# Performance work log

Measured on AMD Instinct MI355X. Metric: run time of the kernel, lower is better.

## Reference

```python
import jax, jax.numpy as jnp
import numpy as np

NUM_EMBEDDINGS = 1024
EMBEDDING_DIM = 64
COMMITMENT_COST = 0.25


def setup_inputs() -> dict:
    key = jax.random.key(0)
    k1, k2 = jax.random.split(key)
    inputs = jax.random.normal(k1, (8, 128, 128, EMBEDDING_DIM), dtype=jnp.float32)
    # nn.Embedding init: uniform(-1/K, 1/K)
    codebook = jax.random.uniform(
        k2, (NUM_EMBEDDINGS, EMBEDDING_DIM), dtype=jnp.float32,
        minval=-1.0 / NUM_EMBEDDINGS, maxval=1.0 / NUM_EMBEDDINGS)
    return {"inputs": inputs, "codebook": codebook}


def reference(inputs, codebook):
    input_shape = inputs.shape
    flat = inputs.reshape(-1, EMBEDDING_DIM)  # [N, D]
    distances = (jnp.sum(flat * flat, axis=1, keepdims=True)
                 + jnp.sum(codebook * codebook, axis=1)
                 - 2.0 * jnp.matmul(flat, codebook.T))  # [N, K]
    encoding_indices = jnp.argmin(distances, axis=1)  # [N]
    # one-hot @ codebook == direct gather
    quantized = codebook[encoding_indices].reshape(input_shape)
    e_latent_loss = jnp.mean((jax.lax.stop_gradient(quantized) - inputs) ** 2)
    q_latent_loss = jnp.mean((quantized - jax.lax.stop_gradient(inputs)) ** 2)
    vq_loss = q_latent_loss + COMMITMENT_COST * e_latent_loss
    # straight-through estimator
    quantized = inputs + jax.lax.stop_gradient(quantized - inputs)
    return (quantized, vq_loss, encoding_indices[:, None])
```

## Files before the change

### kernel.cpp

```cpp
#include <hip/hip_runtime.h>


typedef _Float16 f16x8 __attribute__((ext_vector_type(8)));
typedef float f32x4 __attribute__((ext_vector_type(4)));

constexpr int Dm = 64;
constexpr int Kn = 1024;
constexpr long NR = 131072;
constexpr long QE = NR * (long)Dm;
constexpr int RB = 64;
constexpr int NBLK = (int)(NR / RB);
constexpr int CH = 64;
constexpr int NCH = Kn / CH;
constexpr int SP4 = 17;

constexpr size_t SE_OFF   = 0;
constexpr size_t CBH_OFF  = 4096;
constexpr size_t CNT_OFF  = CBH_OFF + 131072;
constexpr size_t HARD_OFF = CNT_OFF + 256;
constexpr size_t RL_OFF   = HARD_OFF + 4 * 131072;
constexpr size_t PART_OFF = RL_OFF + 4 * 131072;
constexpr size_t WS_REQ   = PART_OFF + 4096;

__global__ __launch_bounds__(256) void vq_prep(const float* __restrict__ cb,
                                               float* __restrict__ se,
                                               _Float16* __restrict__ cbh,
                                               int* __restrict__ cnt)
{
    int j = blockIdx.x * 256 + threadIdx.x;
    const float* e = cb + (size_t)j * Dm;
    _Float16* h = cbh + (size_t)j * Dm;
    float s = 0.f;
    #pragma unroll
    for (int d = 0; d < Dm; ++d) s = fmaf(e[d], e[d], s);
    se[j] = s;
    #pragma unroll
    for (int d = 0; d < Dm; ++d) h[d] = (_Float16)(e[d] * 1024.0f);
    if (j == 0) *cnt = 0;
}

__global__ __launch_bounds__(256, 4) void vq_pass1(
    const float* __restrict__ inp, const float* __restrict__ cb,
    const _Float16* __restrict__ cbh, const float* __restrict__ seg,
    float* __restrict__ out, int* __restrict__ hard_list, int* __restrict__ cnt,
    float* __restrict__ row_loss)
{
    __shared__ __align__(16) _Float16 xh[RB * 72];
    __shared__ float se[Kn];
    __shared__ float gs[RB];
    __shared__ float wm1[4][RB], wm2[4][RB];
    __shared__ int   wi1[4][RB];
    __shared__ int   ridx[RB];
    __shared__ int   easyf[RB];
    __shared__ double qd[RB][4];

    const int tid = threadIdx.x;
    const long rbase = (long)blockIdx.x * RB;

    #pragma unroll
    for (int k = 0; k < 4; ++k) se[tid + 256 * k] = seg[tid + 256 * k];

    {
        const int r = tid >> 2, q = tid & 3;
        const float* src = inp + (rbase + r) * Dm + q * 16;
        _Float16* dst = xh + r * 72 + q * 16;
        #pragma unroll
        for (int i = 0; i < 4; ++i) {
            float4 v = *reinterpret_cast<const float4*>(src + 4 * i);
            dst[4*i+0] = (_Float16)v.x; dst[4*i+1] = (_Float16)v.y;
            dst[4*i+2] = (_Float16)v.z; dst[4*i+3] = (_Float16)v.w;
        }
    }
    if (tid < RB) {
        const float* xr = inp + (rbase + tid) * Dm;
        float g = 0.f;
        #pragma unroll
        for (int d = 0; d < Dm; ++d) g += fabsf(xr[d]);
        gs[tid] = g;
    }
    __syncthreads();

    const int w = tid >> 6, l = tid & 63;
    const int arow = l & 15, kg = l >> 4;

    f16x8 a0[4], a1[4];
    #pragma unroll
    for (int rt = 0; rt < 4; ++rt) {
        const _Float16* ap = xh + (rt * 16 + arow) * 72 + kg * 8;
        a0[rt] = *reinterpret_cast<const f16x8*>(ap);
        a1[rt] = *reinterpret_cast<const f16x8*>(ap + 32);
    }

    float mn1[4][4], mn2[4][4]; int ix1[4][4];
    #pragma unroll
    for (int rt = 0; rt < 4; ++rt)
        #pragma unroll
        for (int r = 0; r < 4; ++r) {
            mn1[rt][r] = __builtin_inff(); mn2[rt][r] = __builtin_inff();
            ix1[rt][r] = 0;
        }

    const int code0 = w * 256 + arow;
    const _Float16* bp = cbh + (size_t)code0 * Dm + kg * 8;

    f16x8 b0 = *reinterpret_cast<const f16x8*>(bp);
    f16x8 b1 = *reinterpret_cast<const f16x8*>(bp + 32);
    #pragma unroll 2
    for (int t = 0; t < 16; ++t) {
        f16x8 c0 = b0, c1 = b1;
        const _Float16* tpn = bp + ((t + 1) & 15) * 16 * Dm;
        b0 = *reinterpret_cast<const f16x8*>(tpn);
        b1 = *reinterpret_cast<const f16x8*>(tpn + 32);
        const int code = code0 + t * 16;
        const float sec = se[code];
        #pragma unroll
        for (int rt = 0; rt < 4; ++rt) {
            f32x4 acc = {0.f, 0.f, 0.f, 0.f};
            acc = __builtin_amdgcn_mfma_f32_16x16x32_f16(a0[rt], c0, acc, 0, 0, 0);
            acc = __builtin_amdgcn_mfma_f32_16x16x32_f16(a1[rt], c1, acc, 0, 0, 0);
            #pragma unroll
            for (int r = 0; r < 4; ++r) {
                float m = fmaf(acc[r], -0.001953125f, sec);
                mn2[rt][r] = fminf(mn2[rt][r], fmaxf(mn1[rt][r], m));
                ix1[rt][r] = (m < mn1[rt][r]) ? code : ix1[rt][r];
                mn1[rt][r] = fminf(mn1[rt][r], m);
            }
        }
    }

    #pragma unroll
    for (int rt = 0; rt < 4; ++rt)
        #pragma unroll
        for (int r = 0; r < 4; ++r) {
            float m1v = mn1[rt][r], m2v = mn2[rt][r]; int i1v = ix1[rt][r];
            #pragma unroll
            for (int off = 1; off < 16; off <<= 1) {
                float om1 = __shfl_xor(m1v, off);
                float om2 = __shfl_xor(m2v, off);
                int   oi1 = __shfl_xor(i1v, off);
                float nm2 = fminf(fminf(m2v, om2), fmaxf(m1v, om1));
                i1v = (om1 < m1v) ? oi1 : i1v;
                m1v = fminf(m1v, om1);
                m2v = nm2;
            }
            if (arow == 0) {
                const int row = rt * 16 + kg * 4 + r;
                wm1[w][row] = m1v; wm2[w][row] = m2v; wi1[w][row] = i1v;
            }
        }
    __syncthreads();

    if (tid < RB) {
        float m1v = wm1[0][tid], m2v = wm2[0][tid]; int i1v = wi1[0][tid];
        #pragma unroll
        for (int q = 1; q < 4; ++q) {
            float am1 = wm1[q][tid], am2 = wm2[q][tid]; int ai = wi1[q][tid];
            float nm2 = fminf(fminf(m2v, am2), fmaxf(m1v, am1));
            i1v = (am1 < m1v) ? ai : i1v;
            m1v = fminf(m1v, am1);
            m2v = nm2;
        }
        const float T = fmaf(gs[tid], 5.2e-6f, 4.0e-5f);
        const int easy = (m2v - m1v) > T;
        ridx[tid] = i1v;
        easyf[tid] = easy;
        if (easy) out[QE + 1 + rbase + tid] = (float)i1v;
        unsigned long long hm = __ballot(!easy);
        const int nh = __popcll(hm);
        int base = 0;
        if (tid == 0 && nh) base = atomicAdd(cnt, nh);
        base = __shfl(base, 0);
        if (!easy) {
            const int pos = base + __popcll(hm & ((1ull << tid) - 1ull));
            hard_list[pos] = (int)(rbase + tid);
        }
    }
    __syncthreads();

    const int r2 = tid >> 2;
    const int dq = (tid & 3) * 16;
    if (easyf[r2]) {
        const long grow = rbase + r2;
        const float* xr2 = inp + grow * (long)Dm + dq;
        const float* q2  = cb + (size_t)ridx[r2] * Dm + dq;
        float* outq = out + grow * (long)Dm + dq;
        double s = 0.0;
        #pragma unroll
        for (int d0 = 0; d0 < 16; d0 += 4) {
            float4 xv = *reinterpret_cast<const float4*>(xr2 + d0);
            float4 qv = *reinterpret_cast<const float4*>(q2 + d0);
            float4 ov;
            float m0 = qv.x - xv.x; ov.x = xv.x + m0;
            float m1 = qv.y - xv.y; ov.y = xv.y + m1;
            float m2 = qv.z - xv.z; ov.z = xv.z + m2;
            float m3 = qv.w - xv.w; ov.w = xv.w + m3;
            s += (double)m0*m0 + (double)m1*m1 + (double)m2*m2 + (double)m3*m3;
            *reinterpret_cast<float4*>(outq + d0) = ov;
        }
        qd[r2][tid & 3] = s;
    }
    __syncthreads();
    if (tid < RB && easyf[tid]) {
        double s = qd[tid][0] + qd[tid][1] + qd[tid][2] + qd[tid][3];
        row_loss[rbase + tid] = (float)s;
    }
}

__global__ __launch_bounds__(256) void vq_pass2(
    const float* __restrict__ inp, const float* __restrict__ cb,
    const float* __restrict__ seg, float* __restrict__ out,
    const int* __restrict__ hard_list, const int* __restrict__ cnt,
    float* __restrict__ row_loss)
{
    __shared__ float4 xs[RB * SP4];
    __shared__ float4 es[CH * SP4];
    __shared__ float  ses[Kn];
    __shared__ float  sxs[RB];
    __shared__ int    hr[RB];
    __shared__ float  bd[RB * 17];
    __shared__ int    bi[RB * 17];
    __shared__ int    comb[RB];
    __shared__ double qd[RB][4];

    const int tid = threadIdx.x;
    const int tr = tid & 15;
    const int tc = tid >> 4;

    #pragma unroll
    for (int k = 0; k < 4; ++k) ses[tid + 256 * k] = seg[tid + 256 * k];

    const int total = *cnt;
    const int nchunk = (total + RB - 1) / RB;
    const float4* gcb = reinterpret_cast<const float4*>(cb);

    for (int c = blockIdx.x; c < nchunk; c += gridDim.x) {
        __syncthreads();
        if (tid < RB) {
            int gi = c * RB + tid;
            hr[tid] = (gi < total) ? hard_list[gi] : -1;
        }
        __syncthreads();

        #pragma unroll
        for (int r = 0; r < 4; ++r) {
            int g = r * 256 + tid;
            int row = g >> 4, col = g & 15;
            int gr = hr[row];
            float4 v = {0.f, 0.f, 0.f, 0.f};
            if (gr >= 0)
                v = *reinterpret_cast<const float4*>(inp + (size_t)gr * Dm + col * 4);
            xs[row * SP4 + col] = v;
        }
        __syncthreads();

        if (tid < RB) {
            const float* xr = reinterpret_cast<const float*>(&xs[tid * SP4]);
            float s = 0.f;
            #pragma unroll
            for (int d = 0; d < Dm; ++d) s = fmaf(xr[d], xr[d], s);
            sxs[tid] = s;
        }
        __syncthreads();

        float sxr[4];
        #pragma unroll
        for (int rr = 0; rr < 4; ++rr) sxr[rr] = sxs[tr + 16 * rr];

        float best[4]; int bidx[4];
        #pragma unroll
        for (int rr = 0; rr < 4; ++rr) { best[rr] = __builtin_inff(); bidx[rr] = 0; }

        for (int ch = 0; ch < NCH; ++ch) {
            __syncthreads();
            #pragma unroll
            for (int r = 0; r < 4; ++r) {
                int g = r * 256 + tid;
                es[(g >> 4) * SP4 + (g & 15)] = gcb[(size_t)ch * (CH * Dm / 4) + g];
            }
            __syncthreads();

            float acc[4][4];
            #pragma unroll
            for (int rr = 0; rr < 4; ++rr)
                #pragma unroll
                for (int cc = 0; cc < 4; ++cc) acc[rr][cc] = 0.f;

            #pragma unroll 4
            for (int db = 0; db < 16; ++db) {
                float4 xf[4], ef[4];
                #pragma unroll
                for (int rr = 0; rr < 4; ++rr) xf[rr] = xs[(tr + 16 * rr) * SP4 + db];
                #pragma unroll
                for (int cc = 0; cc < 4; ++cc) ef[cc] = es[(tc + 16 * cc) * SP4 + db];
                #pragma unroll
                for (int rr = 0; rr < 4; ++rr)
                    #pragma unroll
                    for (int cc = 0; cc < 4; ++cc) {
                        float a = acc[rr][cc];
                        a = fmaf(xf[rr].x, ef[cc].x, a);
                        a = fmaf(xf[rr].y, ef[cc].y, a);
                        a = fmaf(xf[rr].z, ef[cc].z, a);
                        a = fmaf(xf[rr].w, ef[cc].w, a);
                        acc[rr][cc] = a;
                    }
            }

            const int cbase = ch * CH;
            #pragma unroll
            for (int cc = 0; cc < 4; ++cc) {
                const int code = cbase + tc + 16 * cc;
                const float sec = ses[code];
                #pragma unroll
                for (int rr = 0; rr < 4; ++rr) {
                    float dist = (sxr[rr] + sec) - 2.0f * acc[rr][cc];
                    if (dist < best[rr]) { best[rr] = dist; bidx[rr] = code; }
                }
            }
        }

        #pragma unroll
        for (int rr = 0; rr < 4; ++rr) {
            int row = tr + 16 * rr;
            bd[row * 17 + tc] = best[rr];
            bi[row * 17 + tc] = bidx[rr];
        }
        __syncthreads();

        if (tid < RB && hr[tid] >= 0) {
            float b = bd[tid * 17]; int ii = bi[tid * 17];
            #pragma unroll
            for (int q = 1; q < 16; ++q) {
                float d = bd[tid * 17 + q]; int iq = bi[tid * 17 + q];
                if (d < b || (d == b && iq < ii)) { b = d; ii = iq; }
            }
            comb[tid] = ii;
            out[QE + 1 + hr[tid]] = (float)ii;
        }
        __syncthreads();

        const int r2 = tid >> 2;
        const int dq = (tid & 3) * 16;
        if (hr[r2] >= 0) {
            const long grow = hr[r2];
            const float* xr2 = inp + grow * (long)Dm + dq;
            const float* q2  = cb + (size_t)comb[r2] * Dm + dq;
            float* outq = out + grow * (long)Dm + dq;
            double s = 0.0;
            #pragma unroll
            for (int d0 = 0; d0 < 16; d0 += 4) {
                float4 xv = *reinterpret_cast<const float4*>(xr2 + d0);
                float4 qv = *reinterpret_cast<const float4*>(q2 + d0);
                float4 ov;
                float m0 = qv.x - xv.x; ov.x = xv.x + m0;
                float m1 = qv.y - xv.y; ov.y = xv.y + m1;
                float m2 = qv.z - xv.z; ov.z = xv.z + m2;
                float m3 = qv.w - xv.w; ov.w = xv.w + m3;
                s += (double)m0*m0 + (double)m1*m1 + (double)m2*m2 + (double)m3*m3;
                *reinterpret_cast<float4*>(outq + d0) = ov;
            }
            qd[r2][tid & 3] = s;
        }
        __syncthreads();
        if (tid < RB && hr[tid] >= 0) {
            double s = qd[tid][0] + qd[tid][1] + qd[tid][2] + qd[tid][3];
            row_loss[hr[tid]] = (float)s;
        }
    }
}

__global__ __launch_bounds__(256) void vq_lred(const float* __restrict__ row_loss,
                                               double* __restrict__ part)
{
    __shared__ double red[256];
    const int tid = threadIdx.x;
    red[tid] = (double)row_loss[(size_t)blockIdx.x * 256 + tid];
    __syncthreads();
    for (int k = 128; k > 0; k >>= 1) {
        if (tid < k) red[tid] += red[tid + k];
        __syncthreads();
    }
    if (tid == 0) part[blockIdx.x] = red[0];
}

__global__ __launch_bounds__(256) void vq_fin(const double* __restrict__ part,
                                              float* __restrict__ out)
{
    __shared__ double red[256];
    const int tid = threadIdx.x;
    red[tid] = part[tid] + part[tid + 256];
    __syncthreads();
    for (int k = 128; k > 0; k >>= 1) {
        if (tid < k) red[tid] += red[tid + k];
        __syncthreads();
    }
    if (tid == 0) {
        float m = (float)(red[0] / (double)QE);
        out[QE] = m + 0.25f * m;
    }
}

extern "C" void kernel_launch(void* const* d_in, const int* in_sizes, int n_in,
                              void* d_out, int out_size, void* d_ws, size_t ws_size,
                              hipStream_t stream)
{
    const float* inp = (const float*)d_in[0];
    const float* cb  = (const float*)d_in[1];
    float* out = (float*)d_out;
    char* ws = (char*)d_ws;

    float*    se   = (float*)(ws + SE_OFF);
    _Float16* cbh  = (_Float16*)(ws + CBH_OFF);
    int*      cnt  = (int*)(ws + CNT_OFF);
    int*      hard = (int*)(ws + HARD_OFF);
    float*    rl   = (float*)(ws + RL_OFF);
    double*   part = (double*)(ws + PART_OFF);

    vq_prep<<<4, 256, 0, stream>>>(cb, se, cbh, cnt);
    vq_pass1<<<NBLK, 256, 0, stream>>>(inp, cb, cbh, se, out, hard, cnt, rl);
    vq_pass2<<<512, 256, 0, stream>>>(inp, cb, se, out, hard, cnt, rl);
    vq_lred<<<512, 256, 0, stream>>>(rl, part);
    vq_fin<<<1, 256, 0, stream>>>(part, out);
}
```

Measured before the change: 141.5 us.

## Split codebook into fp16 hi/lo parts to tighten pass-1 distance error

The codebook is now stored as a high fp16 part plus a residual low fp16 part, and pass 1 issues two extra MFMAs per tile to add the residual contribution. This halves the approximation error, so the easy/hard margin threshold is halved and fewer rows should fall through to the exact fp32 pass 2. In exchange pass 1 does twice the MFMA work and twice the codebook loads, and it drops the software prefetch of the next B tile.

```diff
diff --git a/kernel.cpp b/kernel.cpp
--- a/kernel.cpp
+++ b/kernel.cpp
@@ -16,7 +16,8 @@
 
 constexpr size_t SE_OFF   = 0;
 constexpr size_t CBH_OFF  = 4096;
-constexpr size_t CNT_OFF  = CBH_OFF + 131072;
+constexpr size_t CBL_OFF  = CBH_OFF + 131072;
+constexpr size_t CNT_OFF  = CBL_OFF + 131072;
 constexpr size_t HARD_OFF = CNT_OFF + 256;
 constexpr size_t RL_OFF   = HARD_OFF + 4 * 131072;
 constexpr size_t PART_OFF = RL_OFF + 4 * 131072;
@@ -25,24 +26,32 @@
 __global__ __launch_bounds__(256) void vq_prep(const float* __restrict__ cb,
                                                float* __restrict__ se,
                                                _Float16* __restrict__ cbh,
+                                               _Float16* __restrict__ cbl,
                                                int* __restrict__ cnt)
 {
     int j = blockIdx.x * 256 + threadIdx.x;
     const float* e = cb + (size_t)j * Dm;
     _Float16* h = cbh + (size_t)j * Dm;
+    _Float16* l = cbl + (size_t)j * Dm;
     float s = 0.f;
     #pragma unroll
     for (int d = 0; d < Dm; ++d) s = fmaf(e[d], e[d], s);
     se[j] = s;
     #pragma unroll
-    for (int d = 0; d < Dm; ++d) h[d] = (_Float16)(e[d] * 1024.0f);
+    for (int d = 0; d < Dm; ++d) {
+        float sc = e[d] * 1024.0f;
+        _Float16 hh = (_Float16)sc;
+        h[d] = hh;
+        l[d] = (_Float16)(sc - (float)hh);
+    }
     if (j == 0) *cnt = 0;
 }
 
 __global__ __launch_bounds__(256, 4) void vq_pass1(
     const float* __restrict__ inp, const float* __restrict__ cb,
-    const _Float16* __restrict__ cbh, const float* __restrict__ seg,
-    float* __restrict__ out, int* __restrict__ hard_list, int* __restrict__ cnt,
+    const _Float16* __restrict__ cbh, const _Float16* __restrict__ cbl,
+    const float* __restrict__ seg, float* __restrict__ out,
+    int* __restrict__ hard_list, int* __restrict__ cnt,
     float* __restrict__ row_loss)
 {
     __shared__ __align__(16) _Float16 xh[RB * 72];
@@ -101,21 +110,24 @@
         }
 
     const int code0 = w * 256 + arow;
-    const _Float16* bp = cbh + (size_t)code0 * Dm + kg * 8;
-
-    f16x8 b0 = *reinterpret_cast<const f16x8*>(bp);
-    f16x8 b1 = *reinterpret_cast<const f16x8*>(bp + 32);
+    const _Float16* bph = cbh + (size_t)code0 * Dm + kg * 8;
+    const _Float16* bpl = cbl + (size_t)code0 * Dm + kg * 8;
+
     #pragma unroll 2
     for (int t = 0; t < 16; ++t) {
-        f16x8 c0 = b0, c1 = b1;
-        const _Float16* tpn = bp + ((t + 1) & 15) * 16 * Dm;
-        b0 = *reinterpret_cast<const f16x8*>(tpn);
-        b1 = *reinterpret_cast<const f16x8*>(tpn + 32);
+        const _Float16* tph = bph + t * 16 * Dm;
+        const _Float16* tpl = bpl + t * 16 * Dm;
+        f16x8 b0 = *reinterpret_cast<const f16x8*>(tph);
+        f16x8 b1 = *reinterpret_cast<const f16x8*>(tph + 32);
+        f16x8 c0 = *reinterpret_cast<const f16x8*>(tpl);
+        f16x8 c1 = *reinterpret_cast<const f16x8*>(tpl + 32);
         const int code = code0 + t * 16;
         const float sec = se[code];
         #pragma unroll
         for (int rt = 0; rt < 4; ++rt) {
             f32x4 acc = {0.f, 0.f, 0.f, 0.f};
+            acc = __builtin_amdgcn_mfma_f32_16x16x32_f16(a0[rt], b0, acc, 0, 0, 0);
+            acc = __builtin_amdgcn_mfma_f32_16x16x32_f16(a1[rt], b1, acc, 0, 0, 0);
             acc = __builtin_amdgcn_mfma_f32_16x16x32_f16(a0[rt], c0, acc, 0, 0, 0);
             acc = __builtin_amdgcn_mfma_f32_16x16x32_f16(a1[rt], c1, acc, 0, 0, 0);
             #pragma unroll
@@ -160,7 +172,7 @@
             m1v = fminf(m1v, am1);
             m2v = nm2;
         }
-        const float T = fmaf(gs[tid], 5.2e-6f, 4.0e-5f);
+        const float T = fmaf(gs[tid], 2.6e-6f, 4.0e-5f);
         const int easy = (m2v - m1v) > T;
         ridx[tid] = i1v;
         easyf[tid] = easy;
@@ -410,13 +422,14 @@
 
     float*    se   = (float*)(ws + SE_OFF);
     _Float16* cbh  = (_Float16*)(ws + CBH_OFF);
+    _Float16* cbl  = (_Float16*)(ws + CBL_OFF);
     int*      cnt  = (int*)(ws + CNT_OFF);
     int*      hard = (int*)(ws + HARD_OFF);
     float*    rl   = (float*)(ws + RL_OFF);
     double*   part = (double*)(ws + PART_OFF);
 
-    vq_prep<<<4, 256, 0, stream>>>(cb, se, cbh, cnt);
-    vq_pass1<<<NBLK, 256, 0, stream>>>(inp, cb, cbh, se, out, hard, cnt, rl);
+    vq_prep<<<4, 256, 0, stream>>>(cb, se, cbh, cbl, cnt);
+    vq_pass1<<<NBLK, 256, 0, stream>>>(inp, cb, cbh, cbl, se, out, hard, cnt, rl);
     vq_pass2<<<512, 256, 0, stream>>>(inp, cb, se, out, hard, cnt, rl);
     vq_lred<<<512, 256, 0, stream>>>(rl, part);
     vq_fin<<<1, 256, 0, stream>>>(part, out);
```

New measurement: 190.4 us. +34.5%, slower.
